# Kernel optimization log

Measured on AMD Instinct MI355X. Metric: run time of the kernel, lower is better.

## Reference

```python
import jax, jax.numpy as jnp
import numpy as np

# Swin block config (matches init_kwargs)
B = 64; H = 28; W = 28; C = 384; NH = 12; WS = 7; SS = 3; HID = 1536
N = WS * WS            # tokens per window (49)
D = C // NH            # head dim (32)
NW = (H // WS) * (W // WS)  # windows per image (16)
SCALE = D ** -0.5


def _rel_pos_index():
    # matches torch.meshgrid default 'ij' indexing
    coords = np.stack(np.meshgrid(np.arange(WS), np.arange(WS), indexing='ij'))
    flat = coords.reshape(2, -1)                      # (2, N)
    rel = flat[:, :, None] - flat[:, None, :]          # (2, N, N)
    rel = rel.transpose(1, 2, 0).copy()                # (N, N, 2)
    rel[:, :, 0] += WS - 1
    rel[:, :, 1] += WS - 1
    rel[:, :, 0] *= 2 * WS - 1
    return rel.sum(-1)                                 # (N, N) int


def _attn_mask():
    img = np.zeros((H, W))
    slices = (slice(0, -WS), slice(-WS, -SS), slice(-SS, None))
    cnt = 0
    for hs in slices:
        for ws in slices:
            img[hs, ws] = cnt
            cnt += 1
    mw = img.reshape(H // WS, WS, W // WS, WS).transpose(0, 2, 1, 3).reshape(-1, N)
    am = mw[:, None, :] - mw[:, :, None]               # (nW, N, N)
    return np.where(am != 0, -100.0, 0.0).astype(np.float32)


def setup_inputs() -> dict:
    key = jax.random.key(0)
    ks = jax.random.split(key, 8)
    p = lambda k, shape: 0.02 * jax.random.normal(k, shape, dtype=jnp.float32)
    return {
        'x_1': jax.random.normal(ks[0], (B, H * W, C), dtype=jnp.float32),
        'act_scaling_factor_1': jnp.ones((1,), jnp.float32),
        'norm1_w': jnp.ones((C,), jnp.float32), 'norm1_b': jnp.zeros((C,), jnp.float32),
        'qkv_w': p(ks[1], (3 * C, C)), 'qkv_b': jnp.zeros((3 * C,), jnp.float32),
        'rel_bias_table': p(ks[2], ((2 * WS - 1) ** 2, NH)),
        'proj_w': p(ks[3], (C, C)), 'proj_b': jnp.zeros((C,), jnp.float32),
        'norm2_w': jnp.ones((C,), jnp.float32), 'norm2_b': jnp.zeros((C,), jnp.float32),
        'fc1_w': p(ks[4], (HID, C)), 'fc1_b': jnp.zeros((HID,), jnp.float32),
        'fc2_w': p(ks[5], (C, HID)), 'fc2_b': jnp.zeros((C,), jnp.float32),
    }


def _ln(x, w, b):
    m = jnp.mean(x, -1, keepdims=True)
    v = jnp.mean((x - m) ** 2, -1, keepdims=True)
    return (x - m) * jax.lax.rsqrt(v + 1e-5) * w + b


def reference(x_1, act_scaling_factor_1, norm1_w, norm1_b, qkv_w, qkv_b,
              rel_bias_table, proj_w, proj_b, norm2_w, norm2_b,
              fc1_w, fc1_b, fc2_w, fc2_b):
    rel_idx = jnp.asarray(_rel_pos_index().reshape(-1))
    mask = jnp.asarray(_attn_mask())
    shortcut = x_1
    h = _ln(x_1, norm1_w, norm1_b).reshape(B, H, W, C)
    h = jnp.roll(h, (-SS, -SS), axis=(1, 2))
    # window partition -> (B*nW, N, C)
    h = h.reshape(B, H // WS, WS, W // WS, WS, C).transpose(0, 1, 3, 2, 4, 5).reshape(-1, N, C)
    qkv = (h @ qkv_w.T + qkv_b).reshape(-1, N, 3, NH, D).transpose(2, 0, 3, 1, 4)
    q, k, v = qkv[0], qkv[1], qkv[2]            # (B_, NH, N, D)
    attn = jnp.einsum('bhnd,bhmd->bhnm', q, k) * SCALE
    bias = rel_bias_table[rel_idx].reshape(N, N, NH).transpose(2, 0, 1)  # (NH, N, N)
    attn = attn + bias[None]
    attn = attn.reshape(B, NW, NH, N, N) + mask[None, :, None]
    attn = jax.nn.softmax(attn.reshape(-1, NH, N, N), axis=-1)
    o = jnp.einsum('bhnm,bhmd->bhnd', attn, v).transpose(0, 2, 1, 3).reshape(-1, N, C)
    o = o @ proj_w.T + proj_b
    # window reverse + unshift
    o = o.reshape(B, H // WS, W // WS, WS, WS, C).transpose(0, 1, 3, 2, 4, 5).reshape(B, H, W, C)
    o = jnp.roll(o, (SS, SS), axis=(1, 2)).reshape(B, H * W, C)
    x2 = shortcut + o
    m = _ln(x2, norm2_w, norm2_b)
    m = jax.nn.gelu(m @ fc1_w.T + fc1_b, approximate=False)
    m = m @ fc2_w.T + fc2_b
    return x2 + m
```

## Files before the change

### kernel.cpp

```cpp
#include <hip/hip_runtime.h>
#include <hip/hip_bf16.h>
#include <math.h>

typedef unsigned short u16;
typedef unsigned int u32;
typedef __attribute__((ext_vector_type(8))) short short8;
typedef __attribute__((ext_vector_type(4))) float f32x4;

__device__ __forceinline__ float b2f(u16 u){ u32 i = ((u32)u)<<16; float f; __builtin_memcpy(&f,&i,4); return f; }
__device__ __forceinline__ u16 f2b(float f){ u32 i; __builtin_memcpy(&i,&f,4); u32 r=(i+0x7FFFu+((i>>16)&1u))>>16; return (u16)r; }
__device__ __forceinline__ int region(int h){ return h<21?0:(h<25?1:2); }

__device__ __forceinline__ int xswz(int bid, int nwg){
  int q = nwg >> 3, r = nwg & 7;
  int xcd = bid & 7, loc = bid >> 3;
  int base = (xcd < r) ? xcd*(q+1) : r*(q+1) + (xcd-r)*q;
  return base + loc;
}

__global__ __launch_bounds__(256) void wcvt_all(
    const float* __restrict__ w0, u16* __restrict__ o0,
    const float* __restrict__ w1, u16* __restrict__ o1,
    const float* __restrict__ w2, u16* __restrict__ o2,
    const float* __restrict__ w3, u16* __restrict__ o3)
{
  int b = blockIdx.x;
  const float* in; u16* out; int ofs;
  if (b < 432){ in=w0; out=o0; ofs=b; }
  else if (b < 576){ in=w1; out=o1; ofs=b-432; }
  else if (b < 1152){ in=w2; out=o2; ofs=b-576; }
  else { in=w3; out=o3; ofs=b-1152; }
  int i = (ofs*256 + threadIdx.x)*4;
  f32x4 v = *(const f32x4*)(in + i);
  u16 o[4];
  #pragma unroll
  for (int e=0;e<4;e++) o[e] = f2b(v[e]);
  *(u32*)(out+i) = (u32)o[0] | ((u32)o[1]<<16);
  *(u32*)(out+i+2) = (u32)o[2] | ((u32)o[3]<<16);
}

__global__ __launch_bounds__(256) void ln1_win(const float* __restrict__ x,
    const float* __restrict__ w, const float* __restrict__ bb, u16* __restrict__ out)
{
  int lane = threadIdx.x & 63;
  int t = blockIdx.x*4 + (threadIdx.x>>6);
  int win = t/49, n = t - win*49;
  int b = win>>4, wi = win&15;
  int r = n/7, c = n - r*7;
  int oh = (wi>>2)*7 + r + 3; if (oh>=28) oh -= 28;
  int ow = (wi&3)*7 + c + 3; if (ow>=28) ow -= 28;
  size_t src = ((size_t)b*784 + oh*28 + ow)*384;
  float v[6];
  #pragma unroll
  for (int p=0;p<3;p++){
    float2 d = *(const float2*)(x + src + 2*lane + 128*p);
    v[2*p] = d.x; v[2*p+1] = d.y;
  }
  float s=0.f, sq=0.f;
  #pragma unroll
  for (int e=0;e<6;e++){ s+=v[e]; sq+=v[e]*v[e]; }
  #pragma unroll
  for (int off=32; off>=1; off>>=1){ s+=__shfl_xor(s,off); sq+=__shfl_xor(sq,off); }
  float mean = s*(1.f/384.f);
  float rstd = rsqrtf(sq*(1.f/384.f)-mean*mean + 1e-5f);
  size_t dst = (size_t)t*384;
  #pragma unroll
  for (int p=0;p<3;p++){
    int col = 2*lane+128*p;
    float2 wd = *(const float2*)(w+col), bd = *(const float2*)(bb+col);
    float y0 = (v[2*p]-mean)*rstd*wd.x + bd.x;
    float y1 = (v[2*p+1]-mean)*rstd*wd.y + bd.y;
    *(u32*)(out + dst + col) = (u32)f2b(y0) | ((u32)f2b(y1)<<16);
  }
}

__global__ __launch_bounds__(256) void ln2_k(const float* __restrict__ x2,
    const float* __restrict__ w, const float* __restrict__ bb, u16* __restrict__ out)
{
  int lane = threadIdx.x & 63;
  int t = blockIdx.x*4 + (threadIdx.x>>6);
  size_t base = (size_t)t*384;
  float v[6];
  #pragma unroll
  for (int p=0;p<3;p++){
    float2 d = *(const float2*)(x2 + base + 2*lane + 128*p);
    v[2*p] = d.x; v[2*p+1] = d.y;
  }
  float s=0.f, sq=0.f;
  #pragma unroll
  for (int e=0;e<6;e++){ s+=v[e]; sq+=v[e]*v[e]; }
  #pragma unroll
  for (int off=32; off>=1; off>>=1){ s+=__shfl_xor(s,off); sq+=__shfl_xor(sq,off); }
  float mean = s*(1.f/384.f);
  float rstd = rsqrtf(sq*(1.f/384.f)-mean*mean + 1e-5f);
  #pragma unroll
  for (int p=0;p<3;p++){
    int col = 2*lane+128*p;
    float2 wd = *(const float2*)(w+col), bd = *(const float2*)(bb+col);
    float y0 = (v[2*p]-mean)*rstd*wd.x + bd.x;
    float y1 = (v[2*p+1]-mean)*rstd*wd.y + bd.y;
    *(u32*)(out + base + col) = (u32)f2b(y0) | ((u32)f2b(y1)<<16);
  }
}

__global__ __launch_bounds__(256) void attn_mfma(const u16* __restrict__ qkv,
    const float* __restrict__ table, u16* __restrict__ out)
{
  __shared__ __align__(16) u16 P[4][4096];
  __shared__ float bsh[4][224];
  int wv = threadIdx.x>>6, lane = threadIdx.x&63;
  int idx = blockIdx.x*4 + wv;
  int winl = idx/12, h = idx - winl*12;
  int wi = winl & 15;
  int g = lane>>4, q15 = lane&15;
  const float SCALE = 0.17677669529663687f;

  for (int e=lane; e<169; e+=64) bsh[wv][e] = table[e*12 + h];

  const u16* base = qkv + (size_t)winl*49*1152 + h*32;

  short8 qa[4], kb[4];
  #pragma unroll
  for (int t=0;t<4;t++){
    int tq = 16*t + q15; if (tq>48) tq = 48;
    qa[t] = *(const short8*)(base + (size_t)tq*1152 + g*8);
    kb[t] = *(const short8*)(base + (size_t)tq*1152 + 384 + g*8);
  }
  f32x4 zero = {0.f,0.f,0.f,0.f};
  f32x4 s[4][4];
  #pragma unroll
  for (int ti=0;ti<4;ti++){
    #pragma unroll
    for (int tj=0;tj<4;tj++) s[ti][tj] = zero;
  }
  #pragma unroll
  for (int ti=0;ti<4;ti++){
    #pragma unroll
    for (int tj=0;tj<4;tj++)
      s[ti][tj] = __builtin_amdgcn_mfma_f32_16x16x32_bf16(qa[ti], kb[tj], s[ti][tj], 0,0,0);
  }

  int hb7 = (wi>>2)*7, wb7 = (wi&3)*7;
  int yj[4], xj[4], ridj[4]; bool kjok[4];
  #pragma unroll
  for (int tj=0;tj<4;tj++){
    int kj = 16*tj + q15;
    kjok[tj] = (kj < 49);
    int y = (kj*37)>>8; int xx = kj - y*7;
    yj[tj] = y; xj[tj] = xx;
    ridj[tj] = region(hb7+y)*3 + region(wb7+xx);
  }
  #pragma unroll
  for (int ti=0;ti<4;ti++){
    #pragma unroll
    for (int r=0;r<4;r++){
      int q = 16*ti + 4*g + r;
      int yi = (q*37)>>8, xi = q - yi*7;
      int ridi = region(hb7+yi)*3 + region(wb7+xi);
      int bb0 = (yi+6)*13 + xi + 6;
      #pragma unroll
      for (int tj=0;tj<4;tj++){
        float v;
        if (kjok[tj]){
          float bias = bsh[wv][bb0 - yj[tj]*13 - xj[tj]];
          v = s[ti][tj][r]*SCALE + bias + ((ridi==ridj[tj]) ? 0.f : -100.f);
        } else v = -1e30f;
        s[ti][tj][r] = v;
      }
    }
  }

  float inv[4][4];
  #pragma unroll
  for (int ti=0;ti<4;ti++){
    #pragma unroll
    for (int r=0;r<4;r++){
      float m = fmaxf(fmaxf(s[ti][0][r], s[ti][1][r]), fmaxf(s[ti][2][r], s[ti][3][r]));
      m = fmaxf(m, __shfl_xor(m,1));
      m = fmaxf(m, __shfl_xor(m,2));
      m = fmaxf(m, __shfl_xor(m,4));
      m = fmaxf(m, __shfl_xor(m,8));
      float sum = 0.f;
      #pragma unroll
      for (int tj=0;tj<4;tj++){
        float e = __expf(s[ti][tj][r] - m);
        s[ti][tj][r] = e; sum += e;
      }
      sum += __shfl_xor(sum,1);
      sum += __shfl_xor(sum,2);
      sum += __shfl_xor(sum,4);
      sum += __shfl_xor(sum,8);
      inv[ti][r] = 1.f/sum;
    }
  }

  u16* Pw = P[wv];
  #pragma unroll
  for (int ti=0;ti<4;ti++){
    #pragma unroll
    for (int r=0;r<4;r++){
      int q = 16*ti + 4*g + r;
      int swz = (q&7)<<4;
      #pragma unroll
      for (int tj=0;tj<4;tj++){
        int kj = 16*tj + q15;
        *(u16*)((char*)Pw + ((q*128 + kj*2) ^ swz)) = f2b(s[ti][tj][r]);
      }
    }
  }
  __syncthreads();

  f32x4 o[4][2];
  #pragma unroll
  for (int ti=0;ti<4;ti++){ o[ti][0]=zero; o[ti][1]=zero; }
  #pragma unroll
  for (int kk=0;kk<2;kk++){
    short8 pa[4];
    #pragma unroll
    for (int ti=0;ti<4;ti++){
      int qq = 16*ti + q15;
      pa[ti] = *(const short8*)((char*)Pw + ((qq*128 + kk*64 + g*16) ^ ((qq&7)<<4)));
    }
    #pragma unroll
    for (int tn=0;tn<2;tn++){
      short8 vb;
      #pragma unroll
      for (int e=0;e<8;e++){
        int tok = kk*32 + g*8 + e; if (tok>48) tok = 48;
        vb[e] = *(const short*)(base + (size_t)tok*1152 + 768 + 16*tn + q15);
      }
      #pragma unroll
      for (int ti=0;ti<4;ti++)
        o[ti][tn] = __builtin_amdgcn_mfma_f32_16x16x32_bf16(pa[ti], vb, o[ti][tn], 0,0,0);
    }
  }

  #pragma unroll
  for (int ti=0;ti<4;ti++){
    #pragma unroll
    for (int r=0;r<4;r++){
      int tok = 16*ti + 4*g + r;
      if (tok < 49){
        float iv = inv[ti][r];
        u16* op = out + ((size_t)(winl*49 + tok))*384 + h*32 + q15;
        op[0]  = f2b(o[ti][0][r]*iv);
        op[16] = f2b(o[ti][1][r]*iv);
      }
    }
  }
}

#define STAGE(b, koff) do { \
  u16* _la = SH + (b)*8192 + wid*512; \
  u16* _lb = SH + (b)*8192 + 4096 + wid*512; \
  __builtin_amdgcn_global_load_lds((const __attribute__((address_space(1))) void*)(gA0+(koff)), \
      (__attribute__((address_space(3))) void*)_la, 16,0,0); \
  __builtin_amdgcn_global_load_lds((const __attribute__((address_space(1))) void*)(gA1+(koff)), \
      (__attribute__((address_space(3))) void*)(_la+2048), 16,0,0); \
  __builtin_amdgcn_global_load_lds((const __attribute__((address_space(1))) void*)(gB0+(koff)), \
      (__attribute__((address_space(3))) void*)_lb, 16,0,0); \
  __builtin_amdgcn_global_load_lds((const __attribute__((address_space(1))) void*)(gB1+(koff)), \
      (__attribute__((address_space(3))) void*)(_lb+2048), 16,0,0); \
} while(0)

#define COMPUTE(b) do { \
  const u16* _Ab = SH + (b)*8192; \
  const u16* _Bb = _Ab + 4096; \
  short8 af[4], bf[4]; \
  _Pragma("unroll") \
  for (int t_=0;t_<4;t_++){ \
    af[t_] = *(const short8*)(_Ab + aidx[t_]); \
    bf[t_] = *(const short8*)(_Bb + bidx[t_]); } \
  __builtin_amdgcn_s_setprio(1); \
  _Pragma("unroll") \
  for (int mi=0;mi<4;mi++){ \
    _Pragma("unroll") \
    for (int ni=0;ni<4;ni++){ \
      acc[mi][ni] = __builtin_amdgcn_mfma_f32_16x16x32_bf16(af[mi], bf[ni], acc[mi][ni], 0,0,0); } } \
  __builtin_amdgcn_s_setprio(0); \
} while(0)

template<int EPI>
__global__ __launch_bounds__(256) void gemm_nt(
    const u16* __restrict__ A, const u16* __restrict__ W,
    const float* __restrict__ bias, u16* __restrict__ outb,
    float* __restrict__ x2, const float* __restrict__ xin,
    float* __restrict__ dout, int rowofs, int N, int K, int ntn)
{
  __shared__ __align__(16) u16 SH[24576];
  int bid = xswz(blockIdx.x, gridDim.x);
  int tm = bid / ntn, tn = bid - tm*ntn;
  int tid = threadIdx.x, lane = tid&63, wid = tid>>6;
  int wm = wid>>1, wn = wid&1;
  int fr = lane&15, fc = lane>>4;

  int s0 = wid*1024 + lane*16;
  int row0 = s0>>6;  int cl0 = ((s0>>4)&3) ^ ((row0>>1)&3);
  int s1b = s0 + 4096;
  int row1 = s1b>>6; int cl1 = ((s1b>>4)&3) ^ ((row1>>1)&3);
  const u16* gA0 = A + (size_t)(tm*128 + row0)*K + cl0*8;
  const u16* gA1 = A + (size_t)(tm*128 + row1)*K + cl1*8;
  const u16* gB0 = W + (size_t)(tn*128 + row0)*K + cl0*8;
  const u16* gB1 = W + (size_t)(tn*128 + row1)*K + cl1*8;

  f32x4 zero = {0.f,0.f,0.f,0.f};
  f32x4 acc[4][4];
  #pragma unroll
  for (int a=0;a<4;a++){
    #pragma unroll
    for (int b=0;b<4;b++) acc[a][b] = zero;
  }
  int aidx[4], bidx[4];
  #pragma unroll
  for (int t_=0;t_<4;t_++){
    int ra = wm*64 + t_*16 + fr;
    aidx[t_] = ra*32 + ((fc ^ ((ra>>1)&3))*8);
    int rb = wn*64 + t_*16 + fr;
    bidx[t_] = rb*32 + ((fc ^ ((rb>>1)&3))*8);
  }

  int NT = K>>5;
  STAGE(0, 0);
  STAGE(1, 32);
  int b = 0;
  for (int t=0; t<NT; ++t){
    if (t < NT-1)  asm volatile("s_waitcnt vmcnt(4)" ::: "memory");
    else           asm volatile("s_waitcnt vmcnt(0)" ::: "memory");
    __builtin_amdgcn_s_barrier();
    __builtin_amdgcn_sched_barrier(0);
    int nb = b+2; if (nb>=3) nb-=3;
    if (t+2 < NT) STAGE(nb, (t+2)*32);
    COMPUTE(b);
    if (++b == 3) b = 0;
  }

  int colbase = tn*128 + wn*64;
  int rowbase = tm*128 + wm*64;

  if (EPI==0 || EPI==2){
    __builtin_amdgcn_s_barrier();
    u16* ep = SH + wid*4096;
    #pragma unroll
    for (int ni=0;ni<4;ni++){
      float bv = bias[colbase + ni*16 + fr];
      #pragma unroll
      for (int mi=0;mi<4;mi++){
        #pragma unroll
        for (int rr=0;rr<4;rr++){
          float v = acc[mi][ni][rr] + bv;
          if (EPI==2){
            float u2 = -1.5957691216057308f*(v + 0.044715f*v*v*v);
            v = v / (1.f + __expf(u2));
          }
          ep[(mi*16 + fc*4 + rr)*64 + ni*16 + fr] = f2b(v);
        }
      }
    }
    int half = lane>>5, c2 = (lane&31)*2;
    #pragma unroll
    for (int it=0; it<32; ++it){
      int lrow = it*2 + half;
      u32 v = *(const u32*)(ep + lrow*64 + c2);
      *(u32*)(outb + (size_t)(rowbase + lrow)*N + colbase + c2) = v;
    }
  } else {
    #pragma unroll
    for (int ni=0;ni<4;ni++){
      int col = colbase + ni*16 + fr;
      float bv = bias[col];
      #pragma unroll
      for (int mi=0;mi<4;mi++){
        #pragma unroll
        for (int rr=0;rr<4;rr++){
          int row = rowbase + mi*16 + fc*4 + rr;
          float v = acc[mi][ni][rr] + bv;
          if (EPI==1){
            int grow = rowofs + row;
            int win = grow/49, n = grow - win*49;
            int bb = win>>4, wi = win&15;
            int hh = (wi>>2)*7 + n/7 + 3; if (hh>=28) hh -= 28;
            int ww = (wi&3)*7 + (n - (n/7)*7) + 3; if (ww>=28) ww -= 28;
            size_t ti = ((size_t)bb*784 + hh*28 + ww)*384 + col;
            x2[ti] = v + xin[ti];
          } else {
            size_t ti = (size_t)row*N + col;
            dout[ti] = v + x2[ti];
          }
        }
      }
    }
  }
}

extern "C" void kernel_launch(void* const* d_in, const int* in_sizes, int n_in,
                              void* d_out, int out_size, void* d_ws, size_t ws_size,
                              hipStream_t stream)
{
  const float* x     = (const float*)d_in[0];
  const float* n1w   = (const float*)d_in[2];
  const float* n1b   = (const float*)d_in[3];
  const float* qkvw  = (const float*)d_in[4];
  const float* qkvb  = (const float*)d_in[5];
  const float* relt  = (const float*)d_in[6];
  const float* projw = (const float*)d_in[7];
  const float* projb = (const float*)d_in[8];
  const float* n2w   = (const float*)d_in[9];
  const float* n2b   = (const float*)d_in[10];
  const float* fc1w  = (const float*)d_in[11];
  const float* fc1b  = (const float*)d_in[12];
  const float* fc2w  = (const float*)d_in[13];
  const float* fc2b  = (const float*)d_in[14];

  int nc;
  if      (ws_size >= 196214784) nc = 1;
  else if (ws_size >= 119144448) nc = 2;
  else                           nc = 4;
  int Mc = 50176/nc;

  char* ws = (char*)d_ws;
  u16* B0    = (u16*)ws;
  u16* qkvc  = (u16*)(ws + 38535168);
  u16* attnc = qkvc + (size_t)Mc*1152;
  u16* fc1c  = qkvc;
  char* wb   = ws + 38535168 + (size_t)Mc*3072;
  u16* wq    = (u16*)(wb);
  u16* wp    = (u16*)(wb + 884736);
  u16* w1    = (u16*)(wb + 1179648);
  u16* w2    = (u16*)(wb + 2359296);
  float* outf = (float*)d_out;

  wcvt_all<<<1728,256,0,stream>>>(qkvw,wq, projw,wp, fc1w,w1, fc2w,w2);

  ln1_win<<<12544,256,0,stream>>>(x, n1w, n1b, B0);

  int mt = Mc/128;
  for (int c=0; c<nc; ++c){
    const u16* a0 = B0 + (size_t)c*Mc*384;
    gemm_nt<0><<<mt*9,256,0,stream>>>(a0, wq, qkvb, qkvc, nullptr, nullptr, nullptr, 0, 1152,384,9);
    attn_mfma<<<Mc/49*3,256,0,stream>>>(qkvc, relt, attnc);
    gemm_nt<1><<<mt*3,256,0,stream>>>(attnc, wp, projb, nullptr, outf, x, nullptr, c*Mc, 384,384,3);
  }

  ln2_k<<<12544,256,0,stream>>>(outf, n2w, n2b, B0);

  for (int c=0; c<nc; ++c){
    const u16* a1 = B0 + (size_t)c*Mc*384;
    float* oc = outf + (size_t)c*Mc*384;
    gemm_nt<2><<<mt*12,256,0,stream>>>(a1, w1, fc1b, fc1c, nullptr, nullptr, nullptr, 0, 1536,384,12);
    gemm_nt<3><<<mt*3 ,256,0,stream>>>(fc1c, w2, fc2b, nullptr, oc, nullptr, oc, 0, 384,1536,3);
  }
}
```

Measured before the change: 452.1 us.

## Fuse FC1, GELU and FC2 into one MLP kernel keeping hidden activations in LDS

Replaces the two MLP GEMM launches, which wrote the 1536-wide GELU activations to global memory and read them back, with a single fused kernel. Each 64-row block loads its LN2 rows into swizzled LDS once, computes FC1 in 128-column chunks, applies GELU into an LDS buffer, and accumulates FC2 into registers before writing the residual output. This removes the large hidden-activation round trip and several launches. In exchange, weight fragments are read straight from global memory with no LDS staging or pipelining, only 784 blocks are launched, and the large accumulator set raises register pressure, which may hurt MFMA throughput.

```diff
diff --git a/kernel.cpp b/kernel.cpp
--- a/kernel.cpp
+++ b/kernel.cpp
@@ -337,7 +337,7 @@
   int colbase = tn*128 + wn*64;
   int rowbase = tm*128 + wm*64;
 
-  if (EPI==0 || EPI==2){
+  if (EPI==0){
     __builtin_amdgcn_s_barrier();
     u16* ep = SH + wid*4096;
     #pragma unroll
@@ -348,10 +348,6 @@
         #pragma unroll
         for (int rr=0;rr<4;rr++){
           float v = acc[mi][ni][rr] + bv;
-          if (EPI==2){
-            float u2 = -1.5957691216057308f*(v + 0.044715f*v*v*v);
-            v = v / (1.f + __expf(u2));
-          }
           ep[(mi*16 + fc*4 + rr)*64 + ni*16 + fr] = f2b(v);
         }
       }
@@ -374,19 +370,126 @@
         for (int rr=0;rr<4;rr++){
           int row = rowbase + mi*16 + fc*4 + rr;
           float v = acc[mi][ni][rr] + bv;
-          if (EPI==1){
-            int grow = rowofs + row;
-            int win = grow/49, n = grow - win*49;
-            int bb = win>>4, wi = win&15;
-            int hh = (wi>>2)*7 + n/7 + 3; if (hh>=28) hh -= 28;
-            int ww = (wi&3)*7 + (n - (n/7)*7) + 3; if (ww>=28) ww -= 28;
-            size_t ti = ((size_t)bb*784 + hh*28 + ww)*384 + col;
-            x2[ti] = v + xin[ti];
-          } else {
-            size_t ti = (size_t)row*N + col;
-            dout[ti] = v + x2[ti];
-          }
+          int grow = rowofs + row;
+          int win = grow/49, n = grow - win*49;
+          int bb = win>>4, wi = win&15;
+          int hh = (wi>>2)*7 + n/7 + 3; if (hh>=28) hh -= 28;
+          int ww = (wi&3)*7 + (n - (n/7)*7) + 3; if (ww>=28) ww -= 28;
+          size_t ti = ((size_t)bb*784 + hh*28 + ww)*384 + col;
+          x2[ti] = v + xin[ti];
         }
+      }
+    }
+  }
+}
+
+__global__ __launch_bounds__(256) void mlp_fused(
+    const u16* __restrict__ A, const u16* __restrict__ w1, const float* __restrict__ b1,
+    const u16* __restrict__ w2, const float* __restrict__ b2, float* __restrict__ io)
+{
+  __shared__ __align__(16) u16 SH[32768];
+  u16* Pb = SH + 24576;
+  int bid = blockIdx.x;
+  int tid = threadIdx.x, lane = tid&63, wn = tid>>6;
+  int fr = lane&15, g = lane>>4;
+
+  #pragma unroll
+  for (int shot=0; shot<12; ++shot){
+    int s = shot*4096 + tid*16;
+    int row = s/768, pb = s - row*768;
+    int lb = pb ^ ((row&7)<<4);
+    const u16* src = A + (size_t)(bid*64+row)*384 + (lb>>1);
+    __builtin_amdgcn_global_load_lds((const __attribute__((address_space(1))) void*)src,
+        (__attribute__((address_space(3))) void*)(SH + (s>>1)), 16,0,0);
+  }
+  asm volatile("s_waitcnt vmcnt(0)" ::: "memory");
+  __builtin_amdgcn_s_barrier();
+
+  f32x4 zero = {0.f,0.f,0.f,0.f};
+  f32x4 acc2[4][6];
+  #pragma unroll
+  for (int mi=0;mi<4;mi++){
+    #pragma unroll
+    for (int ni=0;ni<6;ni++) acc2[mi][ni] = zero;
+  }
+
+  int abase[4], am[4];
+  #pragma unroll
+  for (int mi=0;mi<4;mi++){
+    int ra = mi*16 + fr;
+    abase[mi] = ra*768;
+    am[mi] = (ra&7)<<4;
+  }
+
+  for (int c=0; c<12; ++c){
+    f32x4 acc1[4][2];
+    #pragma unroll
+    for (int mi=0;mi<4;mi++){ acc1[mi][0]=zero; acc1[mi][1]=zero; }
+    const u16* w1base = w1 + (size_t)(c*128 + wn*32 + fr)*384 + g*8;
+    #pragma unroll
+    for (int ks=0; ks<12; ++ks){
+      short8 af[4], bf[2];
+      #pragma unroll
+      for (int mi=0;mi<4;mi++)
+        af[mi] = *(const short8*)((const char*)SH + abase[mi] + ((ks*64 + g*16) ^ am[mi]));
+      bf[0] = *(const short8*)(w1base + ks*32);
+      bf[1] = *(const short8*)(w1base + 16*384 + ks*32);
+      #pragma unroll
+      for (int mi=0;mi<4;mi++){
+        acc1[mi][0] = __builtin_amdgcn_mfma_f32_16x16x32_bf16(af[mi], bf[0], acc1[mi][0], 0,0,0);
+        acc1[mi][1] = __builtin_amdgcn_mfma_f32_16x16x32_bf16(af[mi], bf[1], acc1[mi][1], 0,0,0);
+      }
+    }
+    __builtin_amdgcn_s_barrier();
+    #pragma unroll
+    for (int ni=0;ni<2;ni++){
+      float bv = b1[c*128 + wn*32 + ni*16 + fr];
+      #pragma unroll
+      for (int mi=0;mi<4;mi++){
+        #pragma unroll
+        for (int rr=0;rr<4;rr++){
+          float v = acc1[mi][ni][rr] + bv;
+          float u2 = -1.5957691216057308f*(v + 0.044715f*v*v*v);
+          v = v / (1.f + __expf(u2));
+          int prow = mi*16 + g*4 + rr;
+          int pcol = wn*32 + ni*16 + fr;
+          *(u16*)((char*)Pb + ((prow*256 + pcol*2) ^ ((prow&7)<<4))) = f2b(v);
+        }
+      }
+    }
+    __builtin_amdgcn_s_barrier();
+    const u16* w2base = w2 + (size_t)(wn*96 + fr)*1536 + c*128 + g*8;
+    #pragma unroll
+    for (int ks=0; ks<4; ++ks){
+      short8 pf[4], wf[6];
+      #pragma unroll
+      for (int mi=0;mi<4;mi++){
+        int ra = mi*16 + fr;
+        pf[mi] = *(const short8*)((const char*)Pb + ra*256 + ((ks*64 + g*16) ^ ((ra&7)<<4)));
+      }
+      #pragma unroll
+      for (int ni=0;ni<6;ni++)
+        wf[ni] = *(const short8*)(w2base + (size_t)ni*16*1536 + ks*32);
+      #pragma unroll
+      for (int mi=0;mi<4;mi++){
+        #pragma unroll
+        for (int ni=0;ni<6;ni++)
+          acc2[mi][ni] = __builtin_amdgcn_mfma_f32_16x16x32_bf16(pf[mi], wf[ni], acc2[mi][ni], 0,0,0);
+      }
+    }
+  }
+
+  #pragma unroll
+  for (int ni=0;ni<6;ni++){
+    int col = wn*96 + ni*16 + fr;
+    float bv = b2[col];
+    #pragma unroll
+    for (int mi=0;mi<4;mi++){
+      #pragma unroll
+      for (int rr=0;rr<4;rr++){
+        int row = bid*64 + mi*16 + g*4 + rr;
+        size_t ti = (size_t)row*384 + col;
+        io[ti] = acc2[mi][ni][rr] + bv + io[ti];
       }
     }
   }
@@ -421,7 +524,6 @@
   u16* B0    = (u16*)ws;
   u16* qkvc  = (u16*)(ws + 38535168);
   u16* attnc = qkvc + (size_t)Mc*1152;
-  u16* fc1c  = qkvc;
   char* wb   = ws + 38535168 + (size_t)Mc*3072;
   u16* wq    = (u16*)(wb);
   u16* wp    = (u16*)(wb + 884736);
@@ -443,10 +545,5 @@
 
   ln2_k<<<12544,256,0,stream>>>(outf, n2w, n2b, B0);
 
-  for (int c=0; c<nc; ++c){
-    const u16* a1 = B0 + (size_t)c*Mc*384;
-    float* oc = outf + (size_t)c*Mc*384;
-    gemm_nt<2><<<mt*12,256,0,stream>>>(a1, w1, fc1b, fc1c, nullptr, nullptr, nullptr, 0, 1536,384,12);
-    gemm_nt<3><<<mt*3 ,256,0,stream>>>(fc1c, w2, fc2b, nullptr, oc, nullptr, oc, 0, 384,1536,3);
-  }
-}
+  mlp_fused<<<784,256,0,stream>>>(B0, w1, fc1b, w2, fc2b, outf);
+}
```

After: 681.2 us. +50.7%, slower.

## Store attention residual in bf16 and reschedule large-workspace path

Applied to the files above, without the earlier changes.

When the workspace is large, the proj GEMM epilogue now writes the residual x2 as bf16 into scratch instead of fp32 into the output. A new LayerNorm kernel reads that bf16 buffer, and the fc2 epilogue adds it back from bf16. The attention half runs as a single unchunked pass and the MLP half in two chunks with separate fc1 and attention buffers. This cuts residual memory traffic but rounds the residual to bf16, which loses precision in the final output.

```diff
diff --git a/kernel.cpp b/kernel.cpp
--- a/kernel.cpp
+++ b/kernel.cpp
@@ -85,6 +85,35 @@
   for (int p=0;p<3;p++){
     float2 d = *(const float2*)(x2 + base + 2*lane + 128*p);
     v[2*p] = d.x; v[2*p+1] = d.y;
+  }
+  float s=0.f, sq=0.f;
+  #pragma unroll
+  for (int e=0;e<6;e++){ s+=v[e]; sq+=v[e]*v[e]; }
+  #pragma unroll
+  for (int off=32; off>=1; off>>=1){ s+=__shfl_xor(s,off); sq+=__shfl_xor(sq,off); }
+  float mean = s*(1.f/384.f);
+  float rstd = rsqrtf(sq*(1.f/384.f)-mean*mean + 1e-5f);
+  #pragma unroll
+  for (int p=0;p<3;p++){
+    int col = 2*lane+128*p;
+    float2 wd = *(const float2*)(w+col), bd = *(const float2*)(bb+col);
+    float y0 = (v[2*p]-mean)*rstd*wd.x + bd.x;
+    float y1 = (v[2*p+1]-mean)*rstd*wd.y + bd.y;
+    *(u32*)(out + base + col) = (u32)f2b(y0) | ((u32)f2b(y1)<<16);
+  }
+}
+
+__global__ __launch_bounds__(256) void ln2_b(const u16* __restrict__ x2b,
+    const float* __restrict__ w, const float* __restrict__ bb, u16* __restrict__ out)
+{
+  int lane = threadIdx.x & 63;
+  int t = blockIdx.x*4 + (threadIdx.x>>6);
+  size_t base = (size_t)t*384;
+  float v[6];
+  #pragma unroll
+  for (int p=0;p<3;p++){
+    u32 d = *(const u32*)(x2b + base + 2*lane + 128*p);
+    v[2*p] = b2f((u16)(d&0xFFFFu)); v[2*p+1] = b2f((u16)(d>>16));
   }
   float s=0.f, sq=0.f;
   #pragma unroll
@@ -374,17 +403,21 @@
         for (int rr=0;rr<4;rr++){
           int row = rowbase + mi*16 + fc*4 + rr;
           float v = acc[mi][ni][rr] + bv;
-          if (EPI==1){
+          if (EPI==1 || EPI==4){
             int grow = rowofs + row;
             int win = grow/49, n = grow - win*49;
             int bb = win>>4, wi = win&15;
             int hh = (wi>>2)*7 + n/7 + 3; if (hh>=28) hh -= 28;
             int ww = (wi&3)*7 + (n - (n/7)*7) + 3; if (ww>=28) ww -= 28;
             size_t ti = ((size_t)bb*784 + hh*28 + ww)*384 + col;
-            x2[ti] = v + xin[ti];
+            if (EPI==1) x2[ti] = v + xin[ti];
+            else        outb[ti] = f2b(v + xin[ti]);
+          } else if (EPI==3){
+            size_t ti = (size_t)row*N + col;
+            dout[ti] = v + x2[ti];
           } else {
             size_t ti = (size_t)row*N + col;
-            dout[ti] = v + x2[ti];
+            dout[ti] = v + b2f(outb[ti]);
           }
         }
       }
@@ -411,42 +444,57 @@
   const float* fc2w  = (const float*)d_in[13];
   const float* fc2b  = (const float*)d_in[14];
 
-  int nc;
-  if      (ws_size >= 196214784) nc = 1;
-  else if (ws_size >= 119144448) nc = 2;
-  else                           nc = 4;
-  int Mc = 50176/nc;
-
   char* ws = (char*)d_ws;
-  u16* B0    = (u16*)ws;
-  u16* qkvc  = (u16*)(ws + 38535168);
-  u16* attnc = qkvc + (size_t)Mc*1152;
-  u16* fc1c  = qkvc;
-  char* wb   = ws + 38535168 + (size_t)Mc*3072;
-  u16* wq    = (u16*)(wb);
-  u16* wp    = (u16*)(wb + 884736);
-  u16* w1    = (u16*)(wb + 1179648);
-  u16* w2    = (u16*)(wb + 2359296);
   float* outf = (float*)d_out;
 
-  wcvt_all<<<1728,256,0,stream>>>(qkvw,wq, projw,wp, fc1w,w1, fc2w,w2);
-
-  ln1_win<<<12544,256,0,stream>>>(x, n1w, n1b, B0);
-
-  int mt = Mc/128;
-  for (int c=0; c<nc; ++c){
-    const u16* a0 = B0 + (size_t)c*Mc*384;
-    gemm_nt<0><<<mt*9,256,0,stream>>>(a0, wq, qkvb, qkvc, nullptr, nullptr, nullptr, 0, 1152,384,9);
-    attn_mfma<<<Mc/49*3,256,0,stream>>>(qkvc, relt, attnc);
-    gemm_nt<1><<<mt*3,256,0,stream>>>(attnc, wp, projb, nullptr, outf, x, nullptr, c*Mc, 384,384,3);
-  }
-
-  ln2_k<<<12544,256,0,stream>>>(outf, n2w, n2b, B0);
-
-  for (int c=0; c<nc; ++c){
-    const u16* a1 = B0 + (size_t)c*Mc*384;
-    float* oc = outf + (size_t)c*Mc*384;
-    gemm_nt<2><<<mt*12,256,0,stream>>>(a1, w1, fc1b, fc1c, nullptr, nullptr, nullptr, 0, 1536,384,12);
-    gemm_nt<3><<<mt*3 ,256,0,stream>>>(fc1c, w2, fc2b, nullptr, oc, nullptr, oc, 0, 384,1536,3);
-  }
-}
+  if (ws_size >= 196214784){
+    u16* B0    = (u16*)ws;
+    u16* x2b   = (u16*)(ws + 38535168);
+    u16* qkvc  = (u16*)(ws + 38535168);
+    u16* fc1c  = (u16*)(ws + 77070336);
+    u16* attnc = (u16*)(ws + 154140672);
+    char* wb   = ws + 192675840;
+    u16* wq = (u16*)(wb); u16* wp = (u16*)(wb + 884736);
+    u16* w1 = (u16*)(wb + 1179648); u16* w2 = (u16*)(wb + 2359296);
+
+    wcvt_all<<<1728,256,0,stream>>>(qkvw,wq, projw,wp, fc1w,w1, fc2w,w2);
+    ln1_win<<<12544,256,0,stream>>>(x, n1w, n1b, B0);
+    gemm_nt<0><<<392*9,256,0,stream>>>(B0, wq, qkvb, qkvc, nullptr, nullptr, nullptr, 0, 1152,384,9);
+    attn_mfma<<<3072,256,0,stream>>>(qkvc, relt, attnc);
+    gemm_nt<4><<<392*3,256,0,stream>>>(attnc, wp, projb, x2b, nullptr, x, nullptr, 0, 384,384,3);
+    ln2_b<<<12544,256,0,stream>>>(x2b, n2w, n2b, B0);
+    for (int c=0; c<2; ++c){
+      const u16* a1 = B0 + (size_t)c*25088*384;
+      gemm_nt<2><<<196*12,256,0,stream>>>(a1, w1, fc1b, fc1c, nullptr, nullptr, nullptr, 0, 1536,384,12);
+      gemm_nt<5><<<196*3 ,256,0,stream>>>(fc1c, w2, fc2b, x2b + (size_t)c*25088*384, nullptr, nullptr,
+                                          outf + (size_t)c*25088*384, 0, 384,1536,3);
+    }
+  } else {
+    int nc = (ws_size >= 119144448) ? 2 : 4;
+    int Mc = 50176/nc;
+    u16* B0    = (u16*)ws;
+    u16* qkvc  = (u16*)(ws + 38535168);
+    u16* attnc = qkvc + (size_t)Mc*1152;
+    u16* fc1c  = qkvc;
+    char* wb   = ws + 38535168 + (size_t)Mc*3072;
+    u16* wq = (u16*)(wb); u16* wp = (u16*)(wb + 884736);
+    u16* w1 = (u16*)(wb + 1179648); u16* w2 = (u16*)(wb + 2359296);
+
+    wcvt_all<<<1728,256,0,stream>>>(qkvw,wq, projw,wp, fc1w,w1, fc2w,w2);
+    ln1_win<<<12544,256,0,stream>>>(x, n1w, n1b, B0);
+    int mt = Mc/128;
+    for (int c=0; c<nc; ++c){
+      const u16* a0 = B0 + (size_t)c*Mc*384;
+      gemm_nt<0><<<mt*9,256,0,stream>>>(a0, wq, qkvb, qkvc, nullptr, nullptr, nullptr, 0, 1152,384,9);
+      attn_mfma<<<Mc/49*3,256,0,stream>>>(qkvc, relt, attnc);
+      gemm_nt<1><<<mt*3,256,0,stream>>>(attnc, wp, projb, nullptr, outf, x, nullptr, c*Mc, 384,384,3);
+    }
+    ln2_k<<<12544,256,0,stream>>>(outf, n2w, n2b, B0);
+    for (int c=0; c<nc; ++c){
+      const u16* a1 = B0 + (size_t)c*Mc*384;
+      float* oc = outf + (size_t)c*Mc*384;
+      gemm_nt<2><<<mt*12,256,0,stream>>>(a1, w1, fc1b, fc1c, nullptr, nullptr, nullptr, 0, 1536,384,12);
+      gemm_nt<3><<<mt*3 ,256,0,stream>>>(fc1c, w2, fc2b, nullptr, oc, nullptr, oc, 0, 384,1536,3);
+    }
+  }
+}
```

Result: faster. 434.9 us (-3.8%).
